# Performance work log

Hardware: AMD Instinct MI355X
Metric: run time of the kernel (lower is better)

Reference implementation:

```python
import jax, jax.numpy as jnp
import numpy as np

N = 100000
E = 1600000
F_IN, HID, N_CLS = 128, 16, 32


def setup_inputs() -> dict:
    key = jax.random.key(0)
    ks = jax.random.split(key, 10)
    x = jax.random.normal(ks[0], (N, F_IN), dtype=jnp.float32)
    edge_index = jax.random.randint(ks[1], (2, E), 0, N, dtype=jnp.int64)
    edge_weight = jax.random.uniform(ks[2], (E,), dtype=jnp.float32)
    def glorot(k, shape):
        lim = np.sqrt(6.0 / (shape[0] + shape[1])).astype(np.float32)
        return jax.random.uniform(k, shape, dtype=jnp.float32, minval=-lim, maxval=lim)
    return {
        'x': x, 'edge_index': edge_index, 'edge_weight': edge_weight,
        'W1_0': glorot(ks[3], (F_IN, HID)), 'W1_1': glorot(ks[4], (F_IN, HID)),
        'b1': jnp.zeros((HID,), jnp.float32),
        'W2_0': glorot(ks[5], (HID, N_CLS)), 'W2_1': glorot(ks[6], (HID, N_CLS)),
        'b2': jnp.zeros((N_CLS,), jnp.float32),
    }


def _cheb_conv_k2(x, row, col, edge_weight, W0, W1, b):
    # PyG ChebConv, K=2, lambda_max=2.0:
    #   T0 = x; T1 = L_hat x = D^{-1/2} A D^{-1/2} x - x
    n = x.shape[0]
    deg = jax.ops.segment_sum(edge_weight, row, num_segments=n)  # [N]
    dinv = jnp.where(deg > 0, jax.lax.rsqrt(deg), 0.0)
    norm = dinv[row] * edge_weight * dinv[col]                   # [E]
    agg = jax.ops.segment_sum(norm[:, None] * x[col], row, num_segments=n)  # [N,F]
    tx1 = agg - x
    return x @ W0 + tx1 @ W1 + b


def reference(x, edge_index, edge_weight, W1_0, W1_1, b1, W2_0, W2_1, b2):
    row, col = edge_index[0], edge_index[1]
    h = jax.nn.relu(_cheb_conv_k2(x, row, col, edge_weight, W1_0, W1_1, b1))
    # dropout(p=0) and DFA layers are identity in forward
    out = _cheb_conv_k2(h, row, col, edge_weight, W2_0, W2_1, b2)
    return jax.nn.log_softmax(out, axis=1)
```

## Files before the change

kernel.cpp:

```cpp
#include <hip/hip_runtime.h>
#include <hip/hip_bf16.h>
#include <hip/hip_fp16.h>


constexpr int NN   = 100000;
constexpr int NE   = 1600000;
constexpr int FIN  = 128;
constexpr int HID  = 16;
constexpr int NCLS = 32;

constexpr int RB    = 256;
constexpr int NBKT  = (NN + RB - 1) / RB;
constexpr int EPB   = 4096;
constexpr int EPT   = EPB / 256;
constexpr int GP    = (NE + EPB - 1) / EPB;
constexpr int CAP   = 8192;
constexpr int NTILE = NN / 16;
constexpr int NPAIR = NN / 2;

typedef float f32x2 __attribute__((ext_vector_type(2)));
typedef float f32x4 __attribute__((ext_vector_type(4)));
typedef short bf16x8 __attribute__((ext_vector_type(8)));

#if defined(__has_builtin)
#if __has_builtin(__builtin_amdgcn_cvt_pk_f32_fp8)
#define HAVE_CVT_FP8 1
#endif
#endif

static __device__ __forceinline__ unsigned int f2e4m3(float f) {
    union { float f; unsigned int u; } v; v.f = f;
    unsigned int s = (v.u >> 24) & 0x80u;
    unsigned int au = v.u & 0x7fffffffu;
    if (au > 0x43E00000u) au = 0x43E00000u;
    au += 0x7ffffu + ((au >> 20) & 1u);
    int e4 = (int)(au >> 23) - 120;
    unsigned int m = (au >> 20) & 7u;
    unsigned int byte = (e4 <= 0) ? 0u : (((unsigned int)e4 << 3) | m);
    return s | byte;
}
static __device__ __forceinline__ void fp8x4_fma(unsigned int v, float w, float* acc) {
#ifdef HAVE_CVT_FP8
    f32x2 lo = __builtin_amdgcn_cvt_pk_f32_fp8((int)v, false);
    f32x2 hi = __builtin_amdgcn_cvt_pk_f32_fp8((int)v, true);
    acc[0] += w * lo.x; acc[1] += w * lo.y;
    acc[2] += w * hi.x; acc[3] += w * hi.y;
#else
#pragma unroll
    for (int i = 0; i < 4; i++) {
        unsigned int b = (v >> (8 * i)) & 0xffu;
        float f = __int_as_float((int)(((b & 0x80u) << 24) | ((b & 0x7fu) << 20))) * 0x1p120f;
        acc[i] += w * f;
    }
#endif
}
static __device__ __forceinline__ unsigned short f2bf(float f) {
    union { float f; unsigned int u; } v; v.f = f;
    unsigned int r = v.u + 0x7fffu + ((v.u >> 16) & 1u);
    return (unsigned short)(r >> 16);
}
static __device__ __forceinline__ unsigned int wpack(float wf) {
    unsigned int b = __float_as_uint(wf) + 0x8000u;
    return (b >> 16) & 0x7fffu;
}
static __device__ __forceinline__ float wdec(unsigned int u) {
    return __uint_as_float((u >> 17) << 16);
}

__global__ void k_zero_cur(int* __restrict__ bucketCursor) {
    int i = blockIdx.x * blockDim.x + threadIdx.x;
    if (i < NBKT) bucketCursor[i] = 0;
}

__global__ __launch_bounds__(256) void k_partition(
    const int* __restrict__ row, const int* __restrict__ col,
    const float* __restrict__ w, int* __restrict__ bucketCursor,
    int2* __restrict__ partS) {
    __shared__ int2 stage[EPB];
    __shared__ unsigned short sbkt[EPB];
    __shared__ int cnt[NBKT];
    __shared__ int lofs[NBKT];
    __shared__ int cursor[NBKT];
    __shared__ int gbase[NBKT];
    __shared__ int sa[512], sb[512];
    int tid = threadIdx.x;
    long ebase = (long)blockIdx.x * EPB;
    int rr[EPT]; int cc[EPT]; float wv[EPT];
#pragma unroll
    for (int i = 0; i < EPT; i++) {
        long e = ebase + i * 256 + tid;
        if (e < NE) { rr[i] = row[e]; cc[i] = col[e]; wv[i] = w[e]; }
        else rr[i] = -1;
    }
    for (int i = tid; i < NBKT; i += 256) cnt[i] = 0;
    __syncthreads();
#pragma unroll
    for (int i = 0; i < EPT; i++)
        if (rr[i] >= 0) atomicAdd(&cnt[rr[i] >> 8], 1);
    __syncthreads();
    for (int i = tid; i < 512; i += 256) sa[i] = (i < NBKT) ? cnt[i] : 0;
    __syncthreads();
    int* src = sa; int* dst = sb;
    for (int off = 1; off < 512; off <<= 1) {
        for (int i = tid; i < 512; i += 256)
            dst[i] = src[i] + ((i >= off) ? src[i - off] : 0);
        __syncthreads();
        int* t = src; src = dst; dst = t;
    }
    for (int i = tid; i < NBKT; i += 256) {
        int ex = src[i] - cnt[i];
        lofs[i] = ex;
        cursor[i] = ex;
        int go = (cnt[i] > 0) ? atomicAdd(&bucketCursor[i], cnt[i]) : 0;
        gbase[i] = i * CAP + go;
    }
    __syncthreads();
#pragma unroll
    for (int i = 0; i < EPT; i++) {
        if (rr[i] >= 0) {
            int b = rr[i] >> 8;
            int p = atomicAdd(&cursor[b], 1);
            int2 v;
            v.x = cc[i] | ((rr[i] & 255) << 17);
            v.y = __float_as_int(wv[i]);
            stage[p] = v;
            sbkt[p] = (unsigned short)b;
        }
    }
    __syncthreads();
    int total = (int)min((long)EPB, NE - ebase);
    for (int i = tid; i < total; i += 256) {
        int b = sbkt[i];
        partS[gbase[b] + (i - lofs[b])] = stage[i];
    }
}

__global__ __launch_bounds__(256) void k_bucket_sort_proj1(
    const int2* __restrict__ partS, const int* __restrict__ bucketCursor,
    unsigned int* __restrict__ partC, int* __restrict__ rowptr,
    float* __restrict__ dinv,
    const float* __restrict__ x, const float* __restrict__ W1_0,
    const float* __restrict__ W1_1, const float* __restrict__ b1,
    float* __restrict__ xa, unsigned char* __restrict__ xb8) {
    __shared__ int hist[RB];
    __shared__ int cursor[RB];
    __shared__ float dsum[RB];
    __shared__ float sh_dinv[RB];
    __shared__ int wtot[4];
    __shared__ int red[4];
    int b = blockIdx.x;
    int tid = threadIdx.x;
    int lane = tid & 63, wv = tid >> 6;
    int partial = 0;
    for (int i = tid; i < b; i += 256) partial += bucketCursor[i];
#pragma unroll
    for (int off = 1; off < 64; off <<= 1) partial += __shfl_xor(partial, off, 64);
    if (lane == 0) red[wv] = partial;
    hist[tid] = 0;
    dsum[tid] = 0.f;
    __syncthreads();
    int start = red[0] + red[1] + red[2] + red[3];
    int count = bucketCursor[b];
    const int2* src = partS + (long)b * CAP;
    for (int i = tid; i < count; i += 256)
        atomicAdd(&hist[((unsigned)src[i].x >> 17) & 255], 1);
    __syncthreads();
    int v = hist[tid];
    int sc = v;
#pragma unroll
    for (int off = 1; off < 64; off <<= 1) {
        int up = __shfl_up(sc, off, 64);
        if (lane >= off) sc += up;
    }
    if (lane == 63) wtot[wv] = sc;
    __syncthreads();
    int add = 0;
    for (int w2 = 0; w2 < wv; w2++) add += wtot[w2];
    int ex = sc + add - v;
    int node = b * RB + tid;
    if (node <= NN) rowptr[node] = start + ex;
    cursor[tid] = ex;
    __syncthreads();
    for (int i = tid; i < count; i += 256) {
        int2 p = src[i];
        int rl = ((unsigned)p.x >> 17) & 255;
        int pos = atomicAdd(&cursor[rl], 1);
        float wf = __int_as_float(p.y);
        partC[start + pos] = ((unsigned)p.x & 0x1FFFFu) | (wpack(wf) << 17);
        atomicAdd(&dsum[rl], wf);
    }
    __syncthreads();
    {
        float dsv = dsum[tid];
        float dv = dsv > 0.f ? rsqrtf(dsv) : 0.f;
        if (node < NN) dinv[node] = dv;
        sh_dinv[tid] = dv;
    }
    __syncthreads();

    {
        int pcol = lane & 15, quad = lane >> 4;
        bf16x8 bfrag[2][4];
#pragma unroll
        for (int mat = 0; mat < 2; mat++) {
            const float* W = mat ? W1_1 : W1_0;
#pragma unroll
            for (int kb = 0; kb < 4; kb++) {
                bf16x8 f;
#pragma unroll
                for (int j = 0; j < 8; j++)
                    f[j] = (short)f2bf(W[(kb * 32 + quad * 8 + j) * HID + pcol]);
                bfrag[mat][kb] = f;
            }
        }
        float b1v = b1[pcol];
#pragma unroll
        for (int i = 0; i < 4; i++) {
            int tb = wv * 4 + i;
            int wid = b * 16 + tb;
            if (wid >= NTILE) break;
            const float* xrow = x + ((long)wid * 16 + pcol) * FIN + quad * 8;
            float4 xb[8];
#pragma unroll
            for (int kb = 0; kb < 4; kb++) {
                xb[2 * kb]     = *(const float4*)(xrow + kb * 32);
                xb[2 * kb + 1] = *(const float4*)(xrow + kb * 32 + 4);
            }
            f32x4 acc0 = {0.f, 0.f, 0.f, 0.f}, acc1 = {0.f, 0.f, 0.f, 0.f};
#pragma unroll
            for (int kb = 0; kb < 4; kb++) {
                float4 a0 = xb[2 * kb], a1 = xb[2 * kb + 1];
                bf16x8 af;
                af[0] = (short)f2bf(a0.x); af[1] = (short)f2bf(a0.y);
                af[2] = (short)f2bf(a0.z); af[3] = (short)f2bf(a0.w);
                af[4] = (short)f2bf(a1.x); af[5] = (short)f2bf(a1.y);
                af[6] = (short)f2bf(a1.z); af[7] = (short)f2bf(a1.w);
                acc0 = __builtin_amdgcn_mfma_f32_16x16x32_bf16(af, bfrag[0][kb], acc0, 0, 0, 0);
                acc1 = __builtin_amdgcn_mfma_f32_16x16x32_bf16(af, bfrag[1][kb], acc1, 0, 0, 0);
            }
#pragma unroll
            for (int r = 0; r < 4; r++) {
                int lidx = tb * 16 + quad * 4 + r;
                long nd = (long)b * RB + lidx;
                float a0 = acc0[r], a1 = acc1[r];
                xa[nd * HID + pcol] = a0 - a1 + b1v;
                float dn = sh_dinv[lidx];
                xb8[nd * HID + pcol] = (unsigned char)f2e4m3(dn * a1);
            }
        }
    }
}

__global__ __launch_bounds__(256) void k_gather1(
    const int* __restrict__ rowptr, const unsigned int* __restrict__ partC,
    const float* __restrict__ dinv, const unsigned char* __restrict__ xb8,
    const float* __restrict__ xa,
    unsigned short* __restrict__ h16, unsigned char* __restrict__ h8) {
    long t = (long)blockIdx.x * 256 + threadIdx.x;
    int w = (int)(t >> 6);
    if (w >= NPAIR) return;
    int lane = threadIdx.x & 63;
    int d = lane & 3, p = lane >> 2;
    long n0 = (long)w * 2, n1 = n0 + 1;

    int s0 = rowptr[n0], e0 = rowptr[n0 + 1], e1 = rowptr[n0 + 2];
    float2 dnv = *(const float2*)(dinv + n0);
    float4 xav0 = *(const float4*)(xa + n0 * HID + d * 4);
    float4 xav1 = *(const float4*)(xa + n1 * HID + d * 4);

    float acc0[4] = {0.f, 0.f, 0.f, 0.f};
    float acc1[4] = {0.f, 0.f, 0.f, 0.f};
    int j0 = s0 + p, j1 = e0 + p;
    while ((j0 < e0) | (j1 < e1)) {
        if (j0 < e0) {
            unsigned int u = partC[j0];
            unsigned int v = *(const unsigned int*)(xb8 + (u & 0x1FFFF) * HID + d * 4);
            fp8x4_fma(v, wdec(u), acc0);
            j0 += 16;
        }
        if (j1 < e1) {
            unsigned int u = partC[j1];
            unsigned int v = *(const unsigned int*)(xb8 + (u & 0x1FFFF) * HID + d * 4);
            fp8x4_fma(v, wdec(u), acc1);
            j1 += 16;
        }
    }
#pragma unroll
    for (int i = 0; i < 4; i++) {
        acc0[i] += __shfl_xor(acc0[i], 4);  acc1[i] += __shfl_xor(acc1[i], 4);
        acc0[i] += __shfl_xor(acc0[i], 8);  acc1[i] += __shfl_xor(acc1[i], 8);
        acc0[i] += __shfl_xor(acc0[i], 16); acc1[i] += __shfl_xor(acc1[i], 16);
        acc0[i] += __shfl_xor(acc0[i], 32); acc1[i] += __shfl_xor(acc1[i], 32);
    }
    if (p == 0) {
        float h0[4], h1[4];
        h0[0] = fmaxf(xav0.x + dnv.x * acc0[0], 0.f);
        h0[1] = fmaxf(xav0.y + dnv.x * acc0[1], 0.f);
        h0[2] = fmaxf(xav0.z + dnv.x * acc0[2], 0.f);
        h0[3] = fmaxf(xav0.w + dnv.x * acc0[3], 0.f);
        h1[0] = fmaxf(xav1.x + dnv.y * acc1[0], 0.f);
        h1[1] = fmaxf(xav1.y + dnv.y * acc1[1], 0.f);
        h1[2] = fmaxf(xav1.z + dnv.y * acc1[2], 0.f);
        h1[3] = fmaxf(xav1.w + dnv.y * acc1[3], 0.f);
        ushort4 u0, u1;
        u0.x = f2bf(h0[0]); u0.y = f2bf(h0[1]); u0.z = f2bf(h0[2]); u0.w = f2bf(h0[3]);
        u1.x = f2bf(h1[0]); u1.y = f2bf(h1[1]); u1.z = f2bf(h1[2]); u1.w = f2bf(h1[3]);
        *(ushort4*)(h16 + n0 * HID + d * 4) = u0;
        *(ushort4*)(h16 + n1 * HID + d * 4) = u1;
        unsigned int p0 = f2e4m3(dnv.x * h0[0]) | (f2e4m3(dnv.x * h0[1]) << 8)
                        | (f2e4m3(dnv.x * h0[2]) << 16) | (f2e4m3(dnv.x * h0[3]) << 24);
        unsigned int p1 = f2e4m3(dnv.y * h1[0]) | (f2e4m3(dnv.y * h1[1]) << 8)
                        | (f2e4m3(dnv.y * h1[2]) << 16) | (f2e4m3(dnv.y * h1[3]) << 24);
        *(unsigned int*)(h8 + n0 * HID + d * 4) = p0;
        *(unsigned int*)(h8 + n1 * HID + d * 4) = p1;
    }
}

__global__ __launch_bounds__(256) void k_gather2_lsm(
    const int* __restrict__ rowptr, const unsigned int* __restrict__ partC,
    const float* __restrict__ dinv, const unsigned char* __restrict__ h8,
    const unsigned short* __restrict__ h16,
    const float* __restrict__ W2_0, const float* __restrict__ W2_1,
    const float* __restrict__ b2, float* __restrict__ out) {
    __shared__ unsigned short sh_g[16][16];
    int tile = blockIdx.x;
    int tid = threadIdx.x;
    int lane = tid & 63, wv = tid >> 6;
    int d = lane & 3, p = lane >> 2;
    int nb = tile * 16 + wv * 4;

    int s[5];
#pragma unroll
    for (int k = 0; k < 5; k++) s[k] = rowptr[nb + k];
    float4 dn4 = *(const float4*)(dinv + nb);

    float acc[4][4];
#pragma unroll
    for (int c = 0; c < 4; c++)
#pragma unroll
        for (int i = 0; i < 4; i++) acc[c][i] = 0.f;

    int j0 = s[0] + p, j1 = s[1] + p, j2 = s[2] + p, j3 = s[3] + p;
    int e0 = s[1], e1 = s[2], e2 = s[3], e3 = s[4];
    while ((j0 < e0) | (j1 < e1) | (j2 < e2) | (j3 < e3)) {
        if (j0 < e0) {
            unsigned int u = partC[j0];
            unsigned int v = *(const unsigned int*)(h8 + (u & 0x1FFFF) * HID + d * 4);
            fp8x4_fma(v, wdec(u), acc[0]);
            j0 += 16;
        }
        if (j1 < e1) {
            unsigned int u = partC[j1];
            unsigned int v = *(const unsigned int*)(h8 + (u & 0x1FFFF) * HID + d * 4);
            fp8x4_fma(v, wdec(u), acc[1]);
            j1 += 16;
        }
        if (j2 < e2) {
            unsigned int u = partC[j2];
            unsigned int v = *(const unsigned int*)(h8 + (u & 0x1FFFF) * HID + d * 4);
            fp8x4_fma(v, wdec(u), acc[2]);
            j2 += 16;
        }
        if (j3 < e3) {
            unsigned int u = partC[j3];
            unsigned int v = *(const unsigned int*)(h8 + (u & 0x1FFFF) * HID + d * 4);
            fp8x4_fma(v, wdec(u), acc[3]);
            j3 += 16;
        }
    }
#pragma unroll
    for (int i = 0; i < 4; i++) {
        acc[0][i] += __shfl_xor(acc[0][i], 4);  acc[1][i] += __shfl_xor(acc[1][i], 4);
        acc[2][i] += __shfl_xor(acc[2][i], 4);  acc[3][i] += __shfl_xor(acc[3][i], 4);
        acc[0][i] += __shfl_xor(acc[0][i], 8);  acc[1][i] += __shfl_xor(acc[1][i], 8);
        acc[2][i] += __shfl_xor(acc[2][i], 8);  acc[3][i] += __shfl_xor(acc[3][i], 8);
        acc[0][i] += __shfl_xor(acc[0][i], 16); acc[1][i] += __shfl_xor(acc[1][i], 16);
        acc[2][i] += __shfl_xor(acc[2][i], 16); acc[3][i] += __shfl_xor(acc[3][i], 16);
        acc[0][i] += __shfl_xor(acc[0][i], 32); acc[1][i] += __shfl_xor(acc[1][i], 32);
        acc[2][i] += __shfl_xor(acc[2][i], 32); acc[3][i] += __shfl_xor(acc[3][i], 32);
    }
    if (p == 0) {
        float dnc[4] = {dn4.x, dn4.y, dn4.z, dn4.w};
#pragma unroll
        for (int c = 0; c < 4; c++) {
            ushort4 u;
            u.x = f2bf(dnc[c] * acc[c][0]); u.y = f2bf(dnc[c] * acc[c][1]);
            u.z = f2bf(dnc[c] * acc[c][2]); u.w = f2bf(dnc[c] * acc[c][3]);
            *(ushort4*)&sh_g[wv * 4 + c][d * 4] = u;
        }
    }
    __syncthreads();

    if (wv == 0) {
        int pcol = lane & 15, quad = lane >> 4;
        bf16x8 bfrag[2];
#pragma unroll
        for (int c = 0; c < 2; c++) {
            bf16x8 f;
            if (quad < 2) {
#pragma unroll
                for (int j = 0; j < 8; j++) {
                    int k = quad * 8 + j;
                    f[j] = (short)f2bf(W2_0[k * NCLS + pcol + 16 * c] - W2_1[k * NCLS + pcol + 16 * c]);
                }
            } else {
#pragma unroll
                for (int j = 0; j < 8; j++) {
                    int k = (quad - 2) * 8 + j;
                    f[j] = (short)f2bf(W2_1[k * NCLS + pcol + 16 * c]);
                }
            }
            bfrag[c] = f;
        }
        bf16x8 af;
        if (quad < 2)
            af = *(const bf16x8*)(h16 + ((long)tile * 16 + pcol) * HID + (quad & 1) * 8);
        else
            af = *(const bf16x8*)&sh_g[pcol][(quad & 1) * 8];

        f32x4 c0 = {0.f, 0.f, 0.f, 0.f}, c1 = {0.f, 0.f, 0.f, 0.f};
        c0 = __builtin_amdgcn_mfma_f32_16x16x32_bf16(af, bfrag[0], c0, 0, 0, 0);
        c1 = __builtin_amdgcn_mfma_f32_16x16x32_bf16(af, bfrag[1], c1, 0, 0, 0);

        float b2a = b2[pcol], b2b = b2[pcol + 16];
#pragma unroll
        for (int r = 0; r < 4; r++) {
            long node = (long)tile * 16 + quad * 4 + r;
            float v0 = c0[r] + b2a;
            float v1 = c1[r] + b2b;
            float m = fmaxf(v0, v1);
            m = fmaxf(m, __shfl_xor(m, 1));
            m = fmaxf(m, __shfl_xor(m, 2));
            m = fmaxf(m, __shfl_xor(m, 4));
            m = fmaxf(m, __shfl_xor(m, 8));
            float sum = __expf(v0 - m) + __expf(v1 - m);
            sum += __shfl_xor(sum, 1);
            sum += __shfl_xor(sum, 2);
            sum += __shfl_xor(sum, 4);
            sum += __shfl_xor(sum, 8);
            float ls = logf(sum);
            out[node * NCLS + pcol] = v0 - m - ls;
            out[node * NCLS + pcol + 16] = v1 - m - ls;
        }
    }
}

extern "C" void kernel_launch(void* const* d_in, const int* in_sizes, int n_in,
                              void* d_out, int out_size, void* d_ws, size_t ws_size,
                              hipStream_t stream) {
    const float* x    = (const float*)d_in[0];
    const int*   ei   = (const int*)d_in[1];
    const float* ew   = (const float*)d_in[2];
    const float* W1_0 = (const float*)d_in[3];
    const float* W1_1 = (const float*)d_in[4];
    const float* b1   = (const float*)d_in[5];
    const float* W2_0 = (const float*)d_in[6];
    const float* W2_1 = (const float*)d_in[7];
    const float* b2   = (const float*)d_in[8];
    float* out = (float*)d_out;

    const int* row = ei;
    const int* col = ei + NE;

    char* ws = (char*)d_ws;
    int2*  partS     = (int2*)ws;                 ws += sizeof(int2) * (long)NBKT * CAP;
    unsigned int* partC = (unsigned int*)ws;      ws += sizeof(int) * NE;
    int*   bucketCursor = (int*)ws;               ws += sizeof(int) * NBKT;
    int*   rowptr    = (int*)ws;                  ws += sizeof(int) * (NN + 4);
    float* dinv      = (float*)ws;                ws += sizeof(float) * NN;
    float* xa        = (float*)ws;                ws += sizeof(float) * NN * HID;
    unsigned short* h16 = (unsigned short*)ws;    ws += sizeof(short) * NN * HID;
    unsigned char* xb8 = (unsigned char*)ws;      ws += sizeof(char) * NN * HID;
    unsigned char* h8  = (unsigned char*)ws;      ws += sizeof(char) * NN * HID;

    k_zero_cur<<<(NBKT + 255) / 256, 256, 0, stream>>>(bucketCursor);
    k_partition<<<GP, 256, 0, stream>>>(row, col, ew, bucketCursor, partS);
    k_bucket_sort_proj1<<<NBKT, 256, 0, stream>>>(partS, bucketCursor, partC,
                                                  rowptr, dinv, x, W1_0, W1_1,
                                                  b1, xa, xb8);
    {
        long th = (long)NPAIR * 64;
        k_gather1<<<(int)((th + 255) / 256), 256, 0, stream>>>(
            rowptr, partC, dinv, xb8, xa, h16, h8);
    }
    k_gather2_lsm<<<NTILE, 256, 0, stream>>>(rowptr, partC, dinv, h8, h16,
                                             W2_0, W2_1, b2, out);
}
```

Before: 205.5 us.

## Scatter partition directly to global and process four nodes per wave in gather1

The partition kernel drops its shared-memory staging buffer and prefix-scan, and writes each edge straight to its bucket slot in global memory through a shared per-bucket cursor. This removes the scan and several barriers, but the global stores become scattered instead of contiguous runs per bucket. The layer-1 gather kernel now has each wavefront handle four consecutive nodes instead of two, launched as 16-node tiles like gather2. That should give each lane more independent loads in flight, at the cost of more registers and more divergence when row lengths differ.

```diff
diff --git a/kernel.cpp b/kernel.cpp
--- a/kernel.cpp
+++ b/kernel.cpp
@@ -16,7 +16,6 @@
 constexpr int GP    = (NE + EPB - 1) / EPB;
 constexpr int CAP   = 8192;
 constexpr int NTILE = NN / 16;
-constexpr int NPAIR = NN / 2;
 
 typedef float f32x2 __attribute__((ext_vector_type(2)));
 typedef float f32x4 __attribute__((ext_vector_type(4)));
@@ -76,13 +75,9 @@
     const int* __restrict__ row, const int* __restrict__ col,
     const float* __restrict__ w, int* __restrict__ bucketCursor,
     int2* __restrict__ partS) {
-    __shared__ int2 stage[EPB];
-    __shared__ unsigned short sbkt[EPB];
-    __shared__ int cnt[NBKT];
-    __shared__ int lofs[NBKT];
-    __shared__ int cursor[NBKT];
-    __shared__ int gbase[NBKT];
-    __shared__ int sa[512], sb[512];
+    __shared__ int sh_cnt[NBKT];
+    __shared__ int sh_gbase[NBKT];
+    __shared__ int sh_lcur[NBKT];
     int tid = threadIdx.x;
     long ebase = (long)blockIdx.x * EPB;
     int rr[EPT]; int cc[EPT]; float wv[EPT];
@@ -92,46 +87,27 @@
         if (e < NE) { rr[i] = row[e]; cc[i] = col[e]; wv[i] = w[e]; }
         else rr[i] = -1;
     }
-    for (int i = tid; i < NBKT; i += 256) cnt[i] = 0;
+    for (int i = tid; i < NBKT; i += 256) { sh_cnt[i] = 0; sh_lcur[i] = 0; }
     __syncthreads();
 #pragma unroll
     for (int i = 0; i < EPT; i++)
-        if (rr[i] >= 0) atomicAdd(&cnt[rr[i] >> 8], 1);
-    __syncthreads();
-    for (int i = tid; i < 512; i += 256) sa[i] = (i < NBKT) ? cnt[i] : 0;
-    __syncthreads();
-    int* src = sa; int* dst = sb;
-    for (int off = 1; off < 512; off <<= 1) {
-        for (int i = tid; i < 512; i += 256)
-            dst[i] = src[i] + ((i >= off) ? src[i - off] : 0);
-        __syncthreads();
-        int* t = src; src = dst; dst = t;
-    }
+        if (rr[i] >= 0) atomicAdd(&sh_cnt[rr[i] >> 8], 1);
+    __syncthreads();
     for (int i = tid; i < NBKT; i += 256) {
-        int ex = src[i] - cnt[i];
-        lofs[i] = ex;
-        cursor[i] = ex;
-        int go = (cnt[i] > 0) ? atomicAdd(&bucketCursor[i], cnt[i]) : 0;
-        gbase[i] = i * CAP + go;
+        int c = sh_cnt[i];
+        sh_gbase[i] = i * CAP + ((c > 0) ? atomicAdd(&bucketCursor[i], c) : 0);
     }
     __syncthreads();
 #pragma unroll
     for (int i = 0; i < EPT; i++) {
         if (rr[i] >= 0) {
             int b = rr[i] >> 8;
-            int p = atomicAdd(&cursor[b], 1);
+            int pos = atomicAdd(&sh_lcur[b], 1);
             int2 v;
             v.x = cc[i] | ((rr[i] & 255) << 17);
             v.y = __float_as_int(wv[i]);
-            stage[p] = v;
-            sbkt[p] = (unsigned short)b;
-        }
-    }
-    __syncthreads();
-    int total = (int)min((long)EPB, NE - ebase);
-    for (int i = tid; i < total; i += 256) {
-        int b = sbkt[i];
-        partS[gbase[b] + (i - lofs[b])] = stage[i];
+            partS[sh_gbase[b] + pos] = v;
+        }
     }
 }
 
@@ -256,63 +232,82 @@
     const float* __restrict__ dinv, const unsigned char* __restrict__ xb8,
     const float* __restrict__ xa,
     unsigned short* __restrict__ h16, unsigned char* __restrict__ h8) {
-    long t = (long)blockIdx.x * 256 + threadIdx.x;
-    int w = (int)(t >> 6);
-    if (w >= NPAIR) return;
-    int lane = threadIdx.x & 63;
+    int tile = blockIdx.x;
+    int tid = threadIdx.x;
+    int lane = tid & 63, wv = tid >> 6;
     int d = lane & 3, p = lane >> 2;
-    long n0 = (long)w * 2, n1 = n0 + 1;
-
-    int s0 = rowptr[n0], e0 = rowptr[n0 + 1], e1 = rowptr[n0 + 2];
-    float2 dnv = *(const float2*)(dinv + n0);
-    float4 xav0 = *(const float4*)(xa + n0 * HID + d * 4);
-    float4 xav1 = *(const float4*)(xa + n1 * HID + d * 4);
-
-    float acc0[4] = {0.f, 0.f, 0.f, 0.f};
-    float acc1[4] = {0.f, 0.f, 0.f, 0.f};
-    int j0 = s0 + p, j1 = e0 + p;
-    while ((j0 < e0) | (j1 < e1)) {
+    int nb = tile * 16 + wv * 4;
+
+    int s[5];
+#pragma unroll
+    for (int k = 0; k < 5; k++) s[k] = rowptr[nb + k];
+    float4 dn4 = *(const float4*)(dinv + nb);
+    float4 xav[4];
+#pragma unroll
+    for (int c = 0; c < 4; c++)
+        xav[c] = *(const float4*)(xa + (long)(nb + c) * HID + d * 4);
+
+    float acc[4][4];
+#pragma unroll
+    for (int c = 0; c < 4; c++)
+#pragma unroll
+        for (int i = 0; i < 4; i++) acc[c][i] = 0.f;
+
+    int j0 = s[0] + p, j1 = s[1] + p, j2 = s[2] + p, j3 = s[3] + p;
+    int e0 = s[1], e1 = s[2], e2 = s[3], e3 = s[4];
+    while ((j0 < e0) | (j1 < e1) | (j2 < e2) | (j3 < e3)) {
         if (j0 < e0) {
             unsigned int u = partC[j0];
             unsigned int v = *(const unsigned int*)(xb8 + (u & 0x1FFFF) * HID + d * 4);
-            fp8x4_fma(v, wdec(u), acc0);
+            fp8x4_fma(v, wdec(u), acc[0]);
             j0 += 16;
         }
         if (j1 < e1) {
             unsigned int u = partC[j1];
             unsigned int v = *(const unsigned int*)(xb8 + (u & 0x1FFFF) * HID + d * 4);
-            fp8x4_fma(v, wdec(u), acc1);
+            fp8x4_fma(v, wdec(u), acc[1]);
             j1 += 16;
         }
+        if (j2 < e2) {
+            unsigned int u = partC[j2];
+            unsigned int v = *(const unsigned int*)(xb8 + (u & 0x1FFFF) * HID + d * 4);
+            fp8x4_fma(v, wdec(u), acc[2]);
+            j2 += 16;
+        }
+        if (j3 < e3) {
+            unsigned int u = partC[j3];
+            unsigned int v = *(const unsigned int*)(xb8 + (u & 0x1FFFF) * HID + d * 4);
+            fp8x4_fma(v, wdec(u), acc[3]);
+            j3 += 16;
+        }
     }
 #pragma unroll
     for (int i = 0; i < 4; i++) {
-        acc0[i] += __shfl_xor(acc0[i], 4);  acc1[i] += __shfl_xor(acc1[i], 4);
-        acc0[i] += __shfl_xor(acc0[i], 8);  acc1[i] += __shfl_xor(acc1[i], 8);
-        acc0[i] += __shfl_xor(acc0[i], 16); acc1[i] += __shfl_xor(acc1[i], 16);
-        acc0[i] += __shfl_xor(acc0[i], 32); acc1[i] += __shfl_xor(acc1[i], 32);
+#pragma unroll
+        for (int c = 0; c < 4; c++) acc[c][i] += __shfl_xor(acc[c][i], 4);
+#pragma unroll
+        for (int c = 0; c < 4; c++) acc[c][i] += __shfl_xor(acc[c][i], 8);
+#pragma unroll
+        for (int c = 0; c < 4; c++) acc[c][i] += __shfl_xor(acc[c][i], 16);
+#pragma unroll
+        for (int c = 0; c < 4; c++) acc[c][i] += __shfl_xor(acc[c][i], 32);
     }
     if (p == 0) {
-        float h0[4], h1[4];
-        h0[0] = fmaxf(xav0.x + dnv.x * acc0[0], 0.f);
-        h0[1] = fmaxf(xav0.y + dnv.x * acc0[1], 0.f);
-        h0[2] = fmaxf(xav0.z + dnv.x * acc0[2], 0.f);
-        h0[3] = fmaxf(xav0.w + dnv.x * acc0[3], 0.f);
-        h1[0] = fmaxf(xav1.x + dnv.y * acc1[0], 0.f);
-        h1[1] = fmaxf(xav1.y + dnv.y * acc1[1], 0.f);
-        h1[2] = fmaxf(xav1.z + dnv.y * acc1[2], 0.f);
-        h1[3] = fmaxf(xav1.w + dnv.y * acc1[3], 0.f);
-        ushort4 u0, u1;
-        u0.x = f2bf(h0[0]); u0.y = f2bf(h0[1]); u0.z = f2bf(h0[2]); u0.w = f2bf(h0[3]);
-        u1.x = f2bf(h1[0]); u1.y = f2bf(h1[1]); u1.z = f2bf(h1[2]); u1.w = f2bf(h1[3]);
-        *(ushort4*)(h16 + n0 * HID + d * 4) = u0;
-        *(ushort4*)(h16 + n1 * HID + d * 4) = u1;
-        unsigned int p0 = f2e4m3(dnv.x * h0[0]) | (f2e4m3(dnv.x * h0[1]) << 8)
-                        | (f2e4m3(dnv.x * h0[2]) << 16) | (f2e4m3(dnv.x * h0[3]) << 24);
-        unsigned int p1 = f2e4m3(dnv.y * h1[0]) | (f2e4m3(dnv.y * h1[1]) << 8)
-                        | (f2e4m3(dnv.y * h1[2]) << 16) | (f2e4m3(dnv.y * h1[3]) << 24);
-        *(unsigned int*)(h8 + n0 * HID + d * 4) = p0;
-        *(unsigned int*)(h8 + n1 * HID + d * 4) = p1;
+        float dnc[4] = {dn4.x, dn4.y, dn4.z, dn4.w};
+#pragma unroll
+        for (int c = 0; c < 4; c++) {
+            long n = nb + c;
+            float h0 = fmaxf(xav[c].x + dnc[c] * acc[c][0], 0.f);
+            float h1 = fmaxf(xav[c].y + dnc[c] * acc[c][1], 0.f);
+            float h2 = fmaxf(xav[c].z + dnc[c] * acc[c][2], 0.f);
+            float h3 = fmaxf(xav[c].w + dnc[c] * acc[c][3], 0.f);
+            ushort4 u;
+            u.x = f2bf(h0); u.y = f2bf(h1); u.z = f2bf(h2); u.w = f2bf(h3);
+            *(ushort4*)(h16 + n * HID + d * 4) = u;
+            unsigned int pk = f2e4m3(dnc[c] * h0) | (f2e4m3(dnc[c] * h1) << 8)
+                            | (f2e4m3(dnc[c] * h2) << 16) | (f2e4m3(dnc[c] * h3) << 24);
+            *(unsigned int*)(h8 + n * HID + d * 4) = pk;
+        }
     }
 }
 
@@ -478,11 +473,7 @@
     k_bucket_sort_proj1<<<NBKT, 256, 0, stream>>>(partS, bucketCursor, partC,
                                                   rowptr, dinv, x, W1_0, W1_1,
                                                   b1, xa, xb8);
-    {
-        long th = (long)NPAIR * 64;
-        k_gather1<<<(int)((th + 255) / 256), 256, 0, stream>>>(
-            rowptr, partC, dinv, xb8, xa, h16, h8);
-    }
+    k_gather1<<<NTILE, 256, 0, stream>>>(rowptr, partC, dinv, xb8, xa, h16, h8);
     k_gather2_lsm<<<NTILE, 256, 0, stream>>>(rowptr, partC, dinv, h8, h16,
                                              W2_0, W2_1, b2, out);
 }
```

Result: no change. 209.1 us (+1.7%).
